# Performance work log

Hardware: AMD Instinct MI355X
Metric: run time of the kernel (lower is better)

## Reference

```python
import jax, jax.numpy as jnp
import numpy as np

DMODEL = 2048
HEADS = 16
DHEAD = DMODEL // HEADS  # 128


def setup_inputs() -> dict:
    key = jax.random.key(0)
    ks = jax.random.split(key, 9)
    s = 0.02
    x = jax.random.normal(ks[0], (4, 2048, DMODEL), dtype=jnp.float32)
    Wq = jax.random.normal(ks[1], (DMODEL, DMODEL), dtype=jnp.float32) * s
    bq = jax.random.normal(ks[2], (DMODEL,), dtype=jnp.float32) * s
    Wk = jax.random.normal(ks[3], (DMODEL, DMODEL), dtype=jnp.float32) * s
    bk = jax.random.normal(ks[4], (DMODEL,), dtype=jnp.float32) * s
    Wv = jax.random.normal(ks[5], (DMODEL, DMODEL), dtype=jnp.float32) * s
    bv = jax.random.normal(ks[6], (DMODEL,), dtype=jnp.float32) * s
    Wo = jax.random.normal(ks[7], (DMODEL, DMODEL), dtype=jnp.float32) * s
    bo = jax.random.normal(ks[8], (DMODEL,), dtype=jnp.float32) * s
    return {"x": x, "Wq": Wq, "bq": bq, "Wk": Wk, "bk": bk, "Wv": Wv, "bv": bv, "Wo": Wo, "bo": bo}


def reference(x, Wq, bq, Wk, bk, Wv, bv, Wo, bo):
    b, l, _ = x.shape
    # projections: [b, l, dmodel] -> [b, l, heads, dhead]
    q = (x @ Wq + bq).reshape(b, l, HEADS, DHEAD)
    k = (x @ Wk + bk).reshape(b, l, HEADS, DHEAD)
    v = (x @ Wv + bv).reshape(b, l, HEADS, DHEAD)
    # NOTE: source applies 1/sqrt(dhead) twice -> total scale 1/dhead (faithful)
    a = jnp.einsum('blhd,bLhd->bhlL', q, k) * (1.0 / DHEAD)
    a = jax.nn.softmax(a, axis=-1)
    prefinal = jnp.einsum('bhlL,bLhd->blhd', a, v)
    out = prefinal.reshape(b, l, HEADS * DHEAD) @ Wo + bo
    return out
```

## Files before the change

### kernel.cpp

```cpp
#include <hip/hip_runtime.h>

#define DMODEL 2048
#define SEQ    2048
#define BATCH  4
#define HEADS  16
#define DHEAD  128

typedef __attribute__((ext_vector_type(8))) short short8;
typedef __attribute__((ext_vector_type(4))) float f32x4;
typedef __attribute__((ext_vector_type(16))) float f32x16;

__device__ __forceinline__ unsigned short f2bf(float f) {
  union { float f; unsigned u; } v; v.f = f;
  unsigned r = v.u + 0x7FFFu + ((v.u >> 16) & 1u);
  return (unsigned short)(r >> 16);
}

__global__ __launch_bounds__(256) void cvt_f32_bf16(const float* __restrict__ in,
                                                    unsigned short* __restrict__ out,
                                                    int n4) {
  int i = blockIdx.x * 256 + threadIdx.x;
  if (i >= n4) return;
  float4 v = ((const float4*)in)[i];
  ushort4 o;
  o.x = f2bf(v.x); o.y = f2bf(v.y); o.z = f2bf(v.z); o.w = f2bf(v.w);
  ((ushort4*)out)[i] = o;
}

__global__ __launch_bounds__(256) void transpose_cvt(const float* __restrict__ in,
                                                     unsigned short* __restrict__ out) {
  __shared__ float tile[32][33];
  const int tx = threadIdx.x, ty = threadIdx.y;
  const int x = blockIdx.x * 32 + tx;
  const int y0 = blockIdx.y * 32;
#pragma unroll
  for (int j = 0; j < 32; j += 8)
    tile[ty + j][tx] = in[(size_t)(y0 + ty + j) * DMODEL + x];
  __syncthreads();
  const int xo = blockIdx.y * 32 + tx;
  const int yo0 = blockIdx.x * 32;
#pragma unroll
  for (int j = 0; j < 32; j += 8)
    out[(size_t)(yo0 + ty + j) * DMODEL + xo] = f2bf(tile[tx][ty + j]);
}

__global__ __launch_bounds__(256) void transpose_v(const unsigned short* __restrict__ in,
                                                   unsigned short* __restrict__ out) {
  __shared__ unsigned short t[32][33];
  const int tx = threadIdx.x, ty = threadIdx.y;
  const int bid = blockIdx.x;
  const int lb = bid & 63;
  const int db = (bid >> 6) & 3;
  const int h  = (bid >> 8) & 15;
  const int b  = bid >> 12;
#pragma unroll
  for (int j = 0; j < 32; j += 8)
    t[ty + j][tx] = in[(size_t)(b * SEQ + lb * 32 + ty + j) * DMODEL + h * DHEAD + db * 32 + tx];
  __syncthreads();
  const size_t ob = ((size_t)(b * HEADS + h) * DHEAD + db * 32) * SEQ + lb * 32;
#pragma unroll
  for (int j = 0; j < 32; j += 8)
    out[ob + (size_t)(ty + j) * SEQ + tx] = t[tx][ty + j];
}

template <typename OUT_T>
__global__ __launch_bounds__(256) void gemm_bias(const unsigned short* __restrict__ A,
                                                 const unsigned short* __restrict__ Bt,
                                                 const float* __restrict__ bias,
                                                 OUT_T* __restrict__ C) {
  __shared__ unsigned short As[128 * 32];
  __shared__ unsigned short Bs[128 * 32];
  const int tid = threadIdx.x;
  const int bid = blockIdx.x;
  const int swz = (bid & 7) * 128 + (bid >> 3);
  const int tn = swz & 15;
  const int tm = swz >> 4;
  const int l = tid & 63;
  const int w = tid >> 6;
  const int wr = w >> 1, wc = w & 1;

  const int srow = tid >> 2;
  const int scol = (tid & 3) * 8;
  const unsigned short* Ag = A + (size_t)(tm * 128 + srow) * DMODEL + scol;
  const unsigned short* Bg = Bt + (size_t)(tn * 128 + srow) * DMODEL + scol;
  unsigned short* AsD0 = As + w * 512;
  unsigned short* AsD1 = As + 2048 + w * 512;
  unsigned short* BsD0 = Bs + w * 512;
  unsigned short* BsD1 = Bs + 2048 + w * 512;

  f32x4 acc[4][4] = {};

  for (int k0 = 0; k0 < DMODEL; k0 += 32) {
    __syncthreads();
    __builtin_amdgcn_global_load_lds((const __attribute__((address_space(1))) void*)(Ag + k0),
                                     (__attribute__((address_space(3))) void*)AsD0, 16, 0, 0);
    __builtin_amdgcn_global_load_lds((const __attribute__((address_space(1))) void*)(Ag + (size_t)64 * DMODEL + k0),
                                     (__attribute__((address_space(3))) void*)AsD1, 16, 0, 0);
    __builtin_amdgcn_global_load_lds((const __attribute__((address_space(1))) void*)(Bg + k0),
                                     (__attribute__((address_space(3))) void*)BsD0, 16, 0, 0);
    __builtin_amdgcn_global_load_lds((const __attribute__((address_space(1))) void*)(Bg + (size_t)64 * DMODEL + k0),
                                     (__attribute__((address_space(3))) void*)BsD1, 16, 0, 0);
    __syncthreads();

    short8 af[4], bfr[4];
#pragma unroll
    for (int m = 0; m < 4; ++m)
      af[m] = *(const short8*)&As[(wr * 64 + m * 16 + (l & 15)) * 32 + (l >> 4) * 8];
#pragma unroll
    for (int n = 0; n < 4; ++n)
      bfr[n] = *(const short8*)&Bs[(wc * 64 + n * 16 + (l & 15)) * 32 + (l >> 4) * 8];
#pragma unroll
    for (int m = 0; m < 4; ++m)
#pragma unroll
      for (int n = 0; n < 4; ++n)
        acc[m][n] = __builtin_amdgcn_mfma_f32_16x16x32_bf16(af[m], bfr[n], acc[m][n], 0, 0, 0);
  }

  const int row0 = tm * 128 + wr * 64 + ((l >> 4) * 4);
  const int col0 = tn * 128 + wc * 64 + (l & 15);
#pragma unroll
  for (int n = 0; n < 4; ++n) {
    float bv = bias[col0 + n * 16];
#pragma unroll
    for (int m = 0; m < 4; ++m) {
#pragma unroll
      for (int r = 0; r < 4; ++r) {
        float v = acc[m][n][r] + bv;
        size_t idx = (size_t)(row0 + m * 16 + r) * DMODEL + (col0 + n * 16);
        if constexpr (sizeof(OUT_T) == 2) ((unsigned short*)C)[idx] = f2bf(v);
        else                              ((float*)C)[idx] = v;
      }
    }
  }
}

__global__ __launch_bounds__(256) void attn(const unsigned short* __restrict__ Q,
                                            const unsigned short* __restrict__ K,
                                            const unsigned short* __restrict__ V,
                                            unsigned short* __restrict__ O) {
  __shared__ unsigned short Ks[32 * 136];
  __shared__ unsigned short Vt[128 * 40];
  __shared__ unsigned short Ps[4][16 * 40];

  const int tid = threadIdx.x;
  const int l = tid & 63, w = tid >> 6;
  const int bh = blockIdx.x >> 5, qb = blockIdx.x & 31;
  const int b = bh >> 4, h = bh & 15;
  const size_t base = ((size_t)b * SEQ) * DMODEL + (size_t)h * DHEAD;

  const unsigned short* Qp = Q + base + (size_t)(qb * 64 + w * 16) * DMODEL;
  short8 qf[4];
#pragma unroll
  for (int dc = 0; dc < 4; ++dc)
    qf[dc] = *(const short8*)(Qp + (size_t)(l & 15) * DMODEL + dc * 32 + (l >> 4) * 8);

  f32x4 acc[8] = {};
  float sum[4] = {0.f, 0.f, 0.f, 0.f};

  const int skv = tid >> 3;
  const int sc = (tid & 7) * 16;
  const unsigned short* Kg = K + base + (size_t)skv * DMODEL + sc;
  const unsigned short* Vg = V + base + (size_t)skv * DMODEL + sc;

  const float cexp = 1.4426950408889634f / 128.0f;

  for (int kv0 = 0; kv0 < SEQ; kv0 += 32) {
    __syncthreads();
    short8 ka = *(const short8*)(Kg + (size_t)kv0 * DMODEL);
    short8 kb = *(const short8*)(Kg + (size_t)kv0 * DMODEL + 8);
    *(short8*)&Ks[skv * 136 + sc] = ka;
    *(short8*)&Ks[skv * 136 + sc + 8] = kb;
    short8 va = *(const short8*)(Vg + (size_t)kv0 * DMODEL);
    short8 vb = *(const short8*)(Vg + (size_t)kv0 * DMODEL + 8);
#pragma unroll
    for (int j = 0; j < 8; ++j) {
      Vt[(sc + j) * 40 + skv]     = (unsigned short)va[j];
      Vt[(sc + 8 + j) * 40 + skv] = (unsigned short)vb[j];
    }
    __syncthreads();

    f32x4 s[2];
#pragma unroll
    for (int nh = 0; nh < 2; ++nh) {
      f32x4 t = {};
#pragma unroll
      for (int dc = 0; dc < 4; ++dc) {
        short8 kf = *(const short8*)&Ks[(nh * 16 + (l & 15)) * 136 + dc * 32 + (l >> 4) * 8];
        t = __builtin_amdgcn_mfma_f32_16x16x32_bf16(qf[dc], kf, t, 0, 0, 0);
      }
      s[nh] = t;
    }

#pragma unroll
    for (int nh = 0; nh < 2; ++nh) {
#pragma unroll
      for (int r = 0; r < 4; ++r) {
        float p = exp2f(s[nh][r] * cexp);
        sum[r] += p;
        Ps[w][((l >> 4) * 4 + r) * 40 + (l & 15) + nh * 16] = f2bf(p);
      }
    }

    short8 pf = *(const short8*)&Ps[w][(l & 15) * 40 + (l >> 4) * 8];
#pragma unroll
    for (int db = 0; db < 8; ++db) {
      short8 vf = *(const short8*)&Vt[(db * 16 + (l & 15)) * 40 + (l >> 4) * 8];
      acc[db] = __builtin_amdgcn_mfma_f32_16x16x32_bf16(pf, vf, acc[db], 0, 0, 0);
    }
  }

  float inv[4];
#pragma unroll
  for (int r = 0; r < 4; ++r) {
    float s = sum[r];
    s += __shfl_xor(s, 1);
    s += __shfl_xor(s, 2);
    s += __shfl_xor(s, 4);
    s += __shfl_xor(s, 8);
    inv[r] = 1.0f / s;
  }
  unsigned short* Op = O + base + (size_t)(qb * 64 + w * 16) * DMODEL;
#pragma unroll
  for (int db = 0; db < 8; ++db)
#pragma unroll
    for (int r = 0; r < 4; ++r)
      Op[(size_t)((l >> 4) * 4 + r) * DMODEL + db * 16 + (l & 15)] = f2bf(acc[db][r] * inv[r]);
}

__global__ __launch_bounds__(256, 2) void attn6(const unsigned short* __restrict__ Q,
                                                const unsigned short* __restrict__ K,
                                                const unsigned short* __restrict__ VT,
                                                unsigned short* __restrict__ O) {
  __shared__ unsigned short Ks[2][64 * 128];
  __shared__ unsigned short Vs[2][128 * 64];

  const int tid = threadIdx.x;
  const int l = tid & 63, w = tid >> 6;
  const int x32 = l & 31, h = l >> 5;

  const int bid = blockIdx.x;
  const int swz = (bid & 7) * 64 + (bid >> 3);
  const int bh = swz >> 3, qb = swz & 7;
  const int b = bh >> 4, hh = bh & 15;
  const size_t base = ((size_t)b * SEQ) * DMODEL + (size_t)hh * DHEAD;
  const unsigned short* VTb = VT + (size_t)bh * DHEAD * SEQ;

  const unsigned short* Qp = Q + base + (size_t)(qb * 256 + w * 64) * DMODEL;
  short8 qfA[8], qfB[8];
#pragma unroll
  for (int dc = 0; dc < 8; ++dc) {
    qfA[dc] = *(const short8*)(Qp + (size_t)x32 * DMODEL + dc * 16 + h * 8);
    qfB[dc] = *(const short8*)(Qp + (size_t)(x32 + 32) * DMODEL + dc * 16 + h * 8);
  }

  const unsigned short* Kg0 = K + base + (size_t)(w * 16 + (l >> 4)) * DMODEL + (((l & 15) ^ (l >> 4)) * 8);
  const unsigned short* Kg1 = K + base + (size_t)(w * 16 + (l >> 4)) * DMODEL + (((l & 15) ^ ((l >> 4) + 4)) * 8);
  const unsigned short* Vg0 = VTb + (size_t)(w * 32 + (l >> 3)) * SEQ + (((l & 7) ^ (l >> 3)) * 8);

  unsigned short* KsD = &Ks[0][0];
  unsigned short* VsD = &Vs[0][0];

#define GLL(src, dst) __builtin_amdgcn_global_load_lds( \
    (const __attribute__((address_space(1))) void*)(src), \
    (__attribute__((address_space(3))) void*)(dst), 16, 0, 0)

#define STAGE(bf, kv0) do { \
    GLL(Kg0 + (size_t)(kv0) * DMODEL,        KsD + (bf) * 8192 + w * 2048 + 0 * 512); \
    GLL(Kg1 + (size_t)((kv0) + 4) * DMODEL,  KsD + (bf) * 8192 + w * 2048 + 1 * 512); \
    GLL(Kg0 + (size_t)((kv0) + 8) * DMODEL,  KsD + (bf) * 8192 + w * 2048 + 2 * 512); \
    GLL(Kg1 + (size_t)((kv0) + 12) * DMODEL, KsD + (bf) * 8192 + w * 2048 + 3 * 512); \
    GLL(Vg0 + (size_t)0 * SEQ + (kv0),       VsD + (bf) * 8192 + w * 2048 + 0 * 512); \
    GLL(Vg0 + (size_t)8 * SEQ + (kv0),       VsD + (bf) * 8192 + w * 2048 + 1 * 512); \
    GLL(Vg0 + (size_t)16 * SEQ + (kv0),      VsD + (bf) * 8192 + w * 2048 + 2 * 512); \
    GLL(Vg0 + (size_t)24 * SEQ + (kv0),      VsD + (bf) * 8192 + w * 2048 + 3 * 512); \
  } while (0)

  f32x16 acc0[4] = {}, acc1[4] = {};
  float sum0 = 0.f, sum1 = 0.f;
  const float cexp = 1.4426950408889634f / 128.0f;

#define COMPUTE_SUB(bf, s) do { \
    const unsigned short* Kb_ = &Ks[bf][(s) * 32 * 128]; \
    const unsigned short* Vb_ = &Vs[bf][0]; \
    f32x16 sa0 = {}, sa1 = {}; \
    __builtin_amdgcn_s_setprio(1); \
    _Pragma("unroll") \
    for (int dc = 0; dc < 8; ++dc) { \
      short8 kf = *(const short8*)&Kb_[x32 * 128 + (((dc * 2 + h) ^ (x32 & 7)) * 8)]; \
      sa0 = __builtin_amdgcn_mfma_f32_32x32x16_bf16(kf, qfA[dc], sa0, 0, 0, 0); \
      sa1 = __builtin_amdgcn_mfma_f32_32x32x16_bf16(kf, qfB[dc], sa1, 0, 0, 0); \
    } \
    __builtin_amdgcn_s_setprio(0); \
    union { unsigned u[4]; short8 s8; } pf0A, pf1A, pf0B, pf1B; \
    { \
      float p[16]; \
      _Pragma("unroll") \
      for (int r = 0; r < 16; ++r) { p[r] = __builtin_amdgcn_exp2f(sa0[r] * cexp); sum0 += p[r]; } \
      unsigned pk0[4], pk1[4]; \
      _Pragma("unroll") \
      for (int blk = 0; blk < 4; ++blk) { \
        asm("v_cvt_pk_bf16_f32 %0, %1, %2" : "=v"(pk0[blk]) : "v"(p[blk * 4 + 0]), "v"(p[blk * 4 + 1])); \
        asm("v_cvt_pk_bf16_f32 %0, %1, %2" : "=v"(pk1[blk]) : "v"(p[blk * 4 + 2]), "v"(p[blk * 4 + 3])); \
      } \
      unsigned a0 = pk0[0], a1 = pk0[1], b0 = pk1[0], b1 = pk1[1]; \
      asm("v_permlane32_swap_b32 %0, %1" : "+v"(a0), "+v"(a1)); \
      asm("v_permlane32_swap_b32 %0, %1" : "+v"(b0), "+v"(b1)); \
      pf0A.u[0] = a0; pf0A.u[1] = b0; pf0A.u[2] = a1; pf0A.u[3] = b1; \
      unsigned c0 = pk0[2], c1 = pk0[3], d0 = pk1[2], d1 = pk1[3]; \
      asm("v_permlane32_swap_b32 %0, %1" : "+v"(c0), "+v"(c1)); \
      asm("v_permlane32_swap_b32 %0, %1" : "+v"(d0), "+v"(d1)); \
      pf1A.u[0] = c0; pf1A.u[1] = d0; pf1A.u[2] = c1; pf1A.u[3] = d1; \
    } \
    { \
      float p[16]; \
      _Pragma("unroll") \
      for (int r = 0; r < 16; ++r) { p[r] = __builtin_amdgcn_exp2f(sa1[r] * cexp); sum1 += p[r]; } \
      unsigned pk0[4], pk1[4]; \
      _Pragma("unroll") \
      for (int blk = 0; blk < 4; ++blk) { \
        asm("v_cvt_pk_bf16_f32 %0, %1, %2" : "=v"(pk0[blk]) : "v"(p[blk * 4 + 0]), "v"(p[blk * 4 + 1])); \
        asm("v_cvt_pk_bf16_f32 %0, %1, %2" : "=v"(pk1[blk]) : "v"(p[blk * 4 + 2]), "v"(p[blk * 4 + 3])); \
      } \
      unsigned a0 = pk0[0], a1 = pk0[1], b0 = pk1[0], b1 = pk1[1]; \
      asm("v_permlane32_swap_b32 %0, %1" : "+v"(a0), "+v"(a1)); \
      asm("v_permlane32_swap_b32 %0, %1" : "+v"(b0), "+v"(b1)); \
      pf0B.u[0] = a0; pf0B.u[1] = b0; pf0B.u[2] = a1; pf0B.u[3] = b1; \
      unsigned c0 = pk0[2], c1 = pk0[3], d0 = pk1[2], d1 = pk1[3]; \
      asm("v_permlane32_swap_b32 %0, %1" : "+v"(c0), "+v"(c1)); \
      asm("v_permlane32_swap_b32 %0, %1" : "+v"(d0), "+v"(d1)); \
      pf1B.u[0] = c0; pf1B.u[1] = d0; pf1B.u[2] = c1; pf1B.u[3] = d1; \
    } \
    __builtin_amdgcn_s_setprio(1); \
    _Pragma("unroll") \
    for (int db = 0; db < 4; ++db) { \
      const int row = db * 32 + x32; \
      short8 vf0 = *(const short8*)&Vb_[row * 64 + ((((s) * 4 + 0 + h) ^ (row & 7)) * 8)]; \
      short8 vf1 = *(const short8*)&Vb_[row * 64 + ((((s) * 4 + 2 + h) ^ (row & 7)) * 8)]; \
      acc0[db] = __builtin_amdgcn_mfma_f32_32x32x16_bf16(pf0A.s8, vf0, acc0[db], 0, 0, 0); \
      acc1[db] = __builtin_amdgcn_mfma_f32_32x32x16_bf16(pf0B.s8, vf0, acc1[db], 0, 0, 0); \
      acc0[db] = __builtin_amdgcn_mfma_f32_32x32x16_bf16(pf1A.s8, vf1, acc0[db], 0, 0, 0); \
      acc1[db] = __builtin_amdgcn_mfma_f32_32x32x16_bf16(pf1B.s8, vf1, acc1[db], 0, 0, 0); \
    } \
    __builtin_amdgcn_s_setprio(0); \
  } while (0)

  STAGE(0, 0);
  int buf = 0;
  for (int t = 0; t < 32; ++t) {
    __builtin_amdgcn_s_barrier();
    __builtin_amdgcn_sched_barrier(0);
    if (t < 31) {
      STAGE(buf ^ 1, (t + 1) * 64);
      __builtin_amdgcn_sched_barrier(0);
      asm volatile("s_waitcnt vmcnt(8)" ::: "memory");
    } else {
      asm volatile("s_waitcnt vmcnt(0)" ::: "memory");
    }
    __builtin_amdgcn_sched_barrier(0);
    __builtin_amdgcn_s_barrier();
    __builtin_amdgcn_sched_barrier(0);
    COMPUTE_SUB(buf, 0);
    COMPUTE_SUB(buf, 1);
    buf ^= 1;
  }
#undef COMPUTE_SUB
#undef STAGE
#undef GLL

  sum0 += __shfl_xor(sum0, 32);
  sum1 += __shfl_xor(sum1, 32);
  float inv0 = 1.0f / sum0;
  float inv1 = 1.0f / sum1;
  float invq0[16], invq1[16];
#pragma unroll
  for (int r = 0; r < 16; ++r) {
    const int crow = (r & 3) + 8 * (r >> 2) + 4 * h;
    invq0[r] = __shfl(inv0, crow);
    invq1[r] = __shfl(inv1, crow);
  }

  unsigned short* Op = O + base + (size_t)(qb * 256 + w * 64) * DMODEL;
#pragma unroll
  for (int db = 0; db < 4; ++db)
#pragma unroll
    for (int r = 0; r < 16; ++r) {
      const int crow = (r & 3) + 8 * (r >> 2) + 4 * h;
      Op[(size_t)crow * DMODEL + db * 32 + x32] = f2bf(acc0[db][r] * invq0[r]);
      Op[(size_t)(crow + 32) * DMODEL + db * 32 + x32] = f2bf(acc1[db][r] * invq1[r]);
    }
}

extern "C" void kernel_launch(void* const* d_in, const int* in_sizes, int n_in,
                              void* d_out, int out_size, void* d_ws, size_t ws_size,
                              hipStream_t stream) {
  const float* x  = (const float*)d_in[0];
  const float* Wq = (const float*)d_in[1];
  const float* bq = (const float*)d_in[2];
  const float* Wk = (const float*)d_in[3];
  const float* bk = (const float*)d_in[4];
  const float* Wv = (const float*)d_in[5];
  const float* bv = (const float*)d_in[6];
  const float* Wo = (const float*)d_in[7];
  const float* bo = (const float*)d_in[8];

  char* ws = (char*)d_ws;
  unsigned short* xb  = (unsigned short*)ws;
  unsigned short* WqT = (unsigned short*)(ws + 33554432);
  unsigned short* WkT = (unsigned short*)(ws + 41943040);
  unsigned short* WvT = (unsigned short*)(ws + 50331648);
  unsigned short* WoT = (unsigned short*)(ws + 58720256);
  unsigned short* Qb  = (unsigned short*)(ws + 67108864);
  unsigned short* Kb  = (unsigned short*)(ws + 100663296);
  unsigned short* Vb  = (unsigned short*)(ws + 134217728);
  unsigned short* VTg = (unsigned short*)(ws + 167772160);
  unsigned short* Pf  = xb;

  const bool vt_ok = (ws_size >= (size_t)201326592);

  cvt_f32_bf16<<<16384, 256, 0, stream>>>(x, xb, (BATCH * SEQ * DMODEL) / 4);

  dim3 tb(32, 8), tg(64, 64);
  transpose_cvt<<<tg, tb, 0, stream>>>(Wq, WqT);
  transpose_cvt<<<tg, tb, 0, stream>>>(Wk, WkT);
  transpose_cvt<<<tg, tb, 0, stream>>>(Wv, WvT);
  transpose_cvt<<<tg, tb, 0, stream>>>(Wo, WoT);

  gemm_bias<unsigned short><<<1024, 256, 0, stream>>>(xb, WqT, bq, Qb);
  gemm_bias<unsigned short><<<1024, 256, 0, stream>>>(xb, WkT, bk, Kb);
  gemm_bias<unsigned short><<<1024, 256, 0, stream>>>(xb, WvT, bv, Vb);

  if (vt_ok) {
    transpose_v<<<16384, dim3(32, 8), 0, stream>>>(Vb, VTg);
    attn6<<<512, 256, 0, stream>>>(Qb, Kb, VTg, Pf);
  } else {
    attn<<<2048, 256, 0, stream>>>(Qb, Kb, Vb, Pf);
  }

  gemm_bias<float><<<1024, 256, 0, stream>>>(Pf, WoT, bo, (float*)d_out);
}
```

Measured before the change: 597.9 us.

## Fuse QKV projections into one 256x256-tile double-buffered swizzled GEMM

Replaces the 128x128 single-buffered GEMM with a 512-thread kernel using 256x256 output tiles, a 64-wide K step and double-buffered LDS. Tiles are loaded with direct global-to-LDS copies into an XOR-swizzled layout to avoid LDS bank conflicts, and the next K tile is prefetched while the current one is multiplied. The Q, K and V projections become a single launch that relies on the transposed weights and the output buffers sitting contiguously in the workspace, with the bias picked per column tile. The larger tiles raise data reuse and cut launch count, at the cost of about 128KB of LDS per block and heavy register use, which limits occupancy.

```diff
diff --git a/kernel.cpp b/kernel.cpp
--- a/kernel.cpp
+++ b/kernel.cpp
@@ -63,72 +63,110 @@
     out[ob + (size_t)(ty + j) * SEQ + tx] = t[tx][ty + j];
 }
 
-template <typename OUT_T>
-__global__ __launch_bounds__(256) void gemm_bias(const unsigned short* __restrict__ A,
-                                                 const unsigned short* __restrict__ Bt,
-                                                 const float* __restrict__ bias,
-                                                 OUT_T* __restrict__ C) {
-  __shared__ unsigned short As[128 * 32];
-  __shared__ unsigned short Bs[128 * 32];
+template <typename OUT_T, int NTN>
+__global__ __launch_bounds__(512, 2) void gemm2(const unsigned short* __restrict__ A,
+                                                const unsigned short* __restrict__ Bt,
+                                                const float* __restrict__ b0,
+                                                const float* __restrict__ b1,
+                                                const float* __restrict__ b2,
+                                                OUT_T* __restrict__ C) {
+  __shared__ unsigned short As[2][256 * 64];
+  __shared__ unsigned short Bs[2][256 * 64];
+
   const int tid = threadIdx.x;
+  const int l = tid & 63, w = tid >> 6;
+  const int wr = w >> 2, wc = w & 3;
+
   const int bid = blockIdx.x;
-  const int swz = (bid & 7) * 128 + (bid >> 3);
-  const int tn = swz & 15;
-  const int tm = swz >> 4;
-  const int l = tid & 63;
-  const int w = tid >> 6;
-  const int wr = w >> 1, wc = w & 1;
-
-  const int srow = tid >> 2;
-  const int scol = (tid & 3) * 8;
-  const unsigned short* Ag = A + (size_t)(tm * 128 + srow) * DMODEL + scol;
-  const unsigned short* Bg = Bt + (size_t)(tn * 128 + srow) * DMODEL + scol;
-  unsigned short* AsD0 = As + w * 512;
-  unsigned short* AsD1 = As + 2048 + w * 512;
-  unsigned short* BsD0 = Bs + w * 512;
-  unsigned short* BsD1 = Bs + 2048 + w * 512;
-
-  f32x4 acc[4][4] = {};
-
-  for (int k0 = 0; k0 < DMODEL; k0 += 32) {
-    __syncthreads();
-    __builtin_amdgcn_global_load_lds((const __attribute__((address_space(1))) void*)(Ag + k0),
-                                     (__attribute__((address_space(3))) void*)AsD0, 16, 0, 0);
-    __builtin_amdgcn_global_load_lds((const __attribute__((address_space(1))) void*)(Ag + (size_t)64 * DMODEL + k0),
-                                     (__attribute__((address_space(3))) void*)AsD1, 16, 0, 0);
-    __builtin_amdgcn_global_load_lds((const __attribute__((address_space(1))) void*)(Bg + k0),
-                                     (__attribute__((address_space(3))) void*)BsD0, 16, 0, 0);
-    __builtin_amdgcn_global_load_lds((const __attribute__((address_space(1))) void*)(Bg + (size_t)64 * DMODEL + k0),
-                                     (__attribute__((address_space(3))) void*)BsD1, 16, 0, 0);
-    __syncthreads();
-
-    short8 af[4], bfr[4];
-#pragma unroll
-    for (int m = 0; m < 4; ++m)
-      af[m] = *(const short8*)&As[(wr * 64 + m * 16 + (l & 15)) * 32 + (l >> 4) * 8];
-#pragma unroll
-    for (int n = 0; n < 4; ++n)
-      bfr[n] = *(const short8*)&Bs[(wc * 64 + n * 16 + (l & 15)) * 32 + (l >> 4) * 8];
-#pragma unroll
-    for (int m = 0; m < 4; ++m)
-#pragma unroll
-      for (int n = 0; n < 4; ++n)
-        acc[m][n] = __builtin_amdgcn_mfma_f32_16x16x32_bf16(af[m], bfr[n], acc[m][n], 0, 0, 0);
-  }
-
-  const int row0 = tm * 128 + wr * 64 + ((l >> 4) * 4);
-  const int col0 = tn * 128 + wc * 64 + (l & 15);
+  const int q8 = (32 * NTN) >> 3;
+  const int swz = (bid & 7) * q8 + (bid >> 3);
+  const int tn = swz % NTN;
+  const int tm = swz / NTN;
+
+  const int srow = w * 8 + (l >> 3);
+  const int schunk = (l & 7) ^ (l >> 3);
+  const unsigned short* Ag = A + (size_t)(tm * 256 + srow) * DMODEL + schunk * 8;
+  const unsigned short* Bg = Bt + (size_t)(tn * 256 + srow) * DMODEL + schunk * 8;
+
+#define GLL(src, dst) __builtin_amdgcn_global_load_lds( \
+    (const __attribute__((address_space(1))) void*)(src), \
+    (__attribute__((address_space(3))) void*)(dst), 16, 0, 0)
+
+#define STAGE(bf, kt) do { \
+    GLL(Ag + (size_t)0 * 64 * DMODEL + (kt) * 64,   &As[bf][0 * 4096 + w * 512]); \
+    GLL(Ag + (size_t)1 * 64 * DMODEL + (kt) * 64,   &As[bf][1 * 4096 + w * 512]); \
+    GLL(Ag + (size_t)2 * 64 * DMODEL + (kt) * 64,   &As[bf][2 * 4096 + w * 512]); \
+    GLL(Ag + (size_t)3 * 64 * DMODEL + (kt) * 64,   &As[bf][3 * 4096 + w * 512]); \
+    GLL(Bg + (size_t)0 * 64 * DMODEL + (kt) * 64,   &Bs[bf][0 * 4096 + w * 512]); \
+    GLL(Bg + (size_t)1 * 64 * DMODEL + (kt) * 64,   &Bs[bf][1 * 4096 + w * 512]); \
+    GLL(Bg + (size_t)2 * 64 * DMODEL + (kt) * 64,   &Bs[bf][2 * 4096 + w * 512]); \
+    GLL(Bg + (size_t)3 * 64 * DMODEL + (kt) * 64,   &Bs[bf][3 * 4096 + w * 512]); \
+  } while (0)
+
+  f32x4 acc[8][4] = {};
+
+  STAGE(0, 0);
+  int buf = 0;
+  for (int t = 0; t < 32; ++t) {
+    __builtin_amdgcn_s_barrier();
+    __builtin_amdgcn_sched_barrier(0);
+    if (t < 31) {
+      STAGE(buf ^ 1, t + 1);
+      __builtin_amdgcn_sched_barrier(0);
+      asm volatile("s_waitcnt vmcnt(8)" ::: "memory");
+    } else {
+      asm volatile("s_waitcnt vmcnt(0)" ::: "memory");
+    }
+    __builtin_amdgcn_sched_barrier(0);
+    __builtin_amdgcn_s_barrier();
+    __builtin_amdgcn_sched_barrier(0);
+
+    {
+      const unsigned short* Asb = &As[buf][0];
+      const unsigned short* Bsb = &Bs[buf][0];
+      short8 bfr[4][2];
+#pragma unroll
+      for (int n = 0; n < 4; ++n) {
+        const int row = wc * 64 + n * 16 + (l & 15);
+#pragma unroll
+        for (int ks = 0; ks < 2; ++ks)
+          bfr[n][ks] = *(const short8*)&Bsb[row * 64 + (((ks * 4 + (l >> 4)) ^ (row & 7)) * 8)];
+      }
+      __builtin_amdgcn_s_setprio(1);
+#pragma unroll
+      for (int m = 0; m < 8; ++m) {
+        const int row = wr * 128 + m * 16 + (l & 15);
+        short8 af0 = *(const short8*)&Asb[row * 64 + (((0 + (l >> 4)) ^ (row & 7)) * 8)];
+        short8 af1 = *(const short8*)&Asb[row * 64 + (((4 + (l >> 4)) ^ (row & 7)) * 8)];
+#pragma unroll
+        for (int n = 0; n < 4; ++n) {
+          acc[m][n] = __builtin_amdgcn_mfma_f32_16x16x32_bf16(af0, bfr[n][0], acc[m][n], 0, 0, 0);
+          acc[m][n] = __builtin_amdgcn_mfma_f32_16x16x32_bf16(af1, bfr[n][1], acc[m][n], 0, 0, 0);
+        }
+      }
+      __builtin_amdgcn_s_setprio(0);
+    }
+    buf ^= 1;
+  }
+#undef STAGE
+#undef GLL
+
+  const int bsel = tn >> 3;
+  const float* bp = (bsel == 0) ? b0 : ((bsel == 1) ? b1 : b2);
+  OUT_T* Cb = C + (size_t)bsel * ((size_t)8192 * DMODEL);
+  const int row0 = tm * 256 + wr * 128 + ((l >> 4) * 4);
+  const int lc0 = (tn & 7) * 256 + wc * 64 + (l & 15);
 #pragma unroll
   for (int n = 0; n < 4; ++n) {
-    float bv = bias[col0 + n * 16];
-#pragma unroll
-    for (int m = 0; m < 4; ++m) {
+    float bv = bp[lc0 + n * 16];
+#pragma unroll
+    for (int m = 0; m < 8; ++m) {
 #pragma unroll
       for (int r = 0; r < 4; ++r) {
         float v = acc[m][n][r] + bv;
-        size_t idx = (size_t)(row0 + m * 16 + r) * DMODEL + (col0 + n * 16);
-        if constexpr (sizeof(OUT_T) == 2) ((unsigned short*)C)[idx] = f2bf(v);
-        else                              ((float*)C)[idx] = v;
+        size_t idx = (size_t)(row0 + m * 16 + r) * DMODEL + (lc0 + n * 16);
+        if constexpr (sizeof(OUT_T) == 2) ((unsigned short*)Cb)[idx] = f2bf(v);
+        else                              ((float*)Cb)[idx] = v;
       }
     }
   }
@@ -425,9 +463,7 @@
   transpose_cvt<<<tg, tb, 0, stream>>>(Wv, WvT);
   transpose_cvt<<<tg, tb, 0, stream>>>(Wo, WoT);
 
-  gemm_bias<unsigned short><<<1024, 256, 0, stream>>>(xb, WqT, bq, Qb);
-  gemm_bias<unsigned short><<<1024, 256, 0, stream>>>(xb, WkT, bk, Kb);
-  gemm_bias<unsigned short><<<1024, 256, 0, stream>>>(xb, WvT, bv, Vb);
+  gemm2<unsigned short, 24><<<768, 512, 0, stream>>>(xb, WqT, bq, bk, bv, Qb);
 
   if (vt_ok) {
     transpose_v<<<16384, dim3(32, 8), 0, stream>>>(Vb, VTg);
@@ -436,5 +472,5 @@
     attn<<<2048, 256, 0, stream>>>(Qb, Kb, Vb, Pf);
   }
 
-  gemm_bias<float><<<1024, 256, 0, stream>>>(Pf, WoT, bo, (float*)d_out);
-}
+  gemm2<float, 8><<<256, 512, 0, stream>>>(Pf, WoT, bo, bo, bo, (float*)d_out);
+}
```

Result: faster. 529.6 us (-11.4%).
